# Optimization experiments

Measured on AMD Instinct MI355X. Metric: run time of the kernel, lower is better.

Reference implementation:

```python
import jax, jax.numpy as jnp
import numpy as np

NUM_NODES_G1 = 60000
NUM_NODES_G2 = 50000
NUM_REL = 16
NUM_BASES = 4
DIM = 128  # node_dim == hidden_dim == final_dim
L_COMMON = 100


def _concept_layer(x, edge_index):
    # Gather-based concept propagation: x_i <- x_i + mean_{j in N(i)} x_j
    src, dst = edge_index[0], edge_index[1]
    n = x.shape[0]
    agg = jax.ops.segment_sum(x[src], dst, num_segments=n)
    deg = jax.ops.segment_sum(jnp.ones((src.shape[0],), x.dtype), dst, num_segments=n)
    return x + agg / jnp.clip(deg, 1.0)[:, None]


def _rgcn_layer(x, edge_index, edge_type, basis, comp, root, bias):
    # Basis-decomposed RGCN: out_i = x_i @ root + bias + sum_r (1/|N_i^r|) sum_{j in N_i^r} x_j @ W_r,
    # W_r = sum_b comp[r,b] * basis[b]. Reorder: scatter comp-weighted x[src] per basis, then one GEMM per basis.
    src, dst = edge_index[0], edge_index[1]
    n = x.shape[0]
    e = src.shape[0]
    seg = dst * NUM_REL + edge_type  # per-(node, relation) bucket
    cnt = jax.ops.segment_sum(jnp.ones((e,), x.dtype), seg, num_segments=n * NUM_REL)
    norm = 1.0 / jnp.clip(cnt, 1.0)
    coef = comp[edge_type] * norm[seg][:, None]  # [E, B]
    xsrc = x[src]  # [E, D] -- dominant gather traffic
    out = x @ root + bias
    for b in range(NUM_BASES):  # small fixed loop over bases
        agg_b = jax.ops.segment_sum(xsrc * coef[:, b:b + 1], dst, num_segments=n)
        out = out + agg_b @ basis[b]
    return out


def setup_inputs() -> dict:
    key = jax.random.key(0)
    ks = jax.random.split(key, 16)
    e2, e1 = 800000, 800000
    return {
        "edge_index_g2": jax.random.randint(ks[0], (2, e2), 0, NUM_NODES_G2),
        "edge_type_g2": jax.random.randint(ks[1], (e2,), 0, NUM_REL),
        "edge_index_g1": jax.random.randint(ks[2], (2, e1), 0, NUM_NODES_G1),
        "left_common": jax.random.randint(ks[3], (L_COMMON,), 0, NUM_NODES_G1),
        "all_node_embedding": jax.random.normal(ks[4], (NUM_NODES_G1, DIM), jnp.float32),
        "basis1": jax.random.normal(ks[5], (NUM_BASES, DIM, DIM), jnp.float32) * 0.05,
        "comp1": jax.random.normal(ks[6], (NUM_REL, NUM_BASES), jnp.float32),
        "root1": jax.random.normal(ks[7], (DIM, DIM), jnp.float32) * 0.05,
        "bias1": jnp.zeros((DIM,), jnp.float32),
        "basis2": jax.random.normal(ks[8], (NUM_BASES, DIM, DIM), jnp.float32) * 0.05,
        "comp2": jax.random.normal(ks[9], (NUM_REL, NUM_BASES), jnp.float32),
        "root2": jax.random.normal(ks[10], (DIM, DIM), jnp.float32) * 0.05,
        "bias2": jnp.zeros((DIM,), jnp.float32),
        "weights": jax.random.uniform(ks[11], (DIM, 1), jnp.float32),
    }


def reference(edge_index_g2, edge_type_g2, edge_index_g1, left_common,
              all_node_embedding, basis1, comp1, root1, bias1,
              basis2, comp2, root2, bias2, weights):
    x_g1 = jax.nn.relu(_concept_layer(all_node_embedding, edge_index_g1))
    x = x_g1[:NUM_NODES_G2]
    x = _rgcn_layer(x, edge_index_g2, edge_type_g2, basis1, comp1, root1, bias1)
    x = jax.nn.relu(x)  # relu_use == 1
    x_g2 = _rgcn_layer(x, edge_index_g2, edge_type_g2, basis2, comp2, root2, bias2)
    ty = x_g1[left_common]  # [L, D]
    # mul_def outer elementwise product followed by matmul with weights collapses to one contraction:
    # logits[n,l] = sum_d x_g2[n,d] * ty[l,d] * w[d]
    logits = jnp.einsum('nd,ld,d->nl', x_g2, ty, weights[:, 0])
    return jax.nn.softmax(logits, axis=1)
```

## Files before the change

### kernel.cpp

```cpp
#include <hip/hip_runtime.h>
#include <hip/hip_bf16.h>
#include <math.h>

#define N1 60000
#define N2 50000
#define DIM 128
#define NREL 16
#define NB 4
#define LCOM 100
#define LPAD 112
#define NPART 8

typedef __attribute__((ext_vector_type(8))) short short8;
typedef __attribute__((ext_vector_type(4))) float f32x4;
typedef __attribute__((ext_vector_type(4))) _Float16 half4;
typedef __attribute__((ext_vector_type(8))) _Float16 half8;

__device__ __forceinline__ float bf2f(unsigned short u) {
    union { unsigned int i; float f; } c; c.i = ((unsigned int)u) << 16; return c.f;
}
__device__ __forceinline__ unsigned short f2bf(float f) {
    union { float f; unsigned int i; } c; c.f = f;
    unsigned int r = c.i + 0x7FFF + ((c.i >> 16) & 1);
    return (unsigned short)(r >> 16);
}
__device__ __forceinline__ void split8(float4 a, float4 b, short8& h, short8& l) {
    float f[8] = {a.x, a.y, a.z, a.w, b.x, b.y, b.z, b.w};
#pragma unroll
    for (int j = 0; j < 8; j++) {
        unsigned short hh = f2bf(f[j]);
        h[j] = (short)hh;
        l[j] = (short)f2bf(f[j] - bf2f(hh));
    }
}

__global__ __launch_bounds__(256) void k_prelude(
        const int* __restrict__ ei1, int E1, int* __restrict__ deg1, int HB1,
        const int* __restrict__ ei2, int E2, int* __restrict__ deg2, int HB2,
        const float* __restrict__ root1, const float* __restrict__ basis1,
        unsigned short* __restrict__ Wh1, unsigned short* __restrict__ Wl1,
        const float* __restrict__ root2, const float* __restrict__ basis2,
        unsigned short* __restrict__ Wh2, unsigned short* __restrict__ Wl2, int PB,
        const float* __restrict__ emb, _Float16* __restrict__ embh, int n4) {
    int b = blockIdx.x;
    if (b < HB1) {
        int e0 = b * 1024 + threadIdx.x;
#pragma unroll
        for (int j = 0; j < 4; j++) {
            int e = e0 + j * 256;
            if (e < E1) atomicAdd(deg1 + __builtin_nontemporal_load(ei1 + E1 + e), 1);
        }
    } else if (b < HB1 + HB2) {
        int e0 = (b - HB1) * 1024 + threadIdx.x;
#pragma unroll
        for (int j = 0; j < 4; j++) {
            int e = e0 + j * 256;
            if (e < E2) atomicAdd(deg2 + __builtin_nontemporal_load(ei2 + E2 + e), 1);
        }
    } else if (b < HB1 + HB2 + PB) {
        int t = (b - HB1 - HB2) * 256 + threadIdx.x;
        if (t < 2 * 640 * 128) {
            int which = t >= 640 * 128;
            int tt = which ? t - 640 * 128 : t;
            const float* root = which ? root2 : root1;
            const float* basis = which ? basis2 : basis1;
            unsigned short* Wh = which ? Wh2 : Wh1;
            unsigned short* Wl = which ? Wl2 : Wl1;
            int k = tt >> 7, n = tt & 127;
            float v = (k < 128) ? root[k * 128 + n] : basis[(k - 128) * 128 + n];
            unsigned short h = f2bf(v);
            Wh[n * 640 + k] = h;
            Wl[n * 640 + k] = f2bf(v - bf2f(h));
        }
    } else {
        int i = (b - HB1 - HB2 - PB) * 256 + threadIdx.x;
        if (i < n4) {
            float4 v = ((const float4*)emb)[i];
            half4 o = {(_Float16)v.x, (_Float16)v.y, (_Float16)v.z, (_Float16)v.w};
            ((half4*)embh)[i] = o;
        }
    }
}

__global__ __launch_bounds__(256) void k_scan_p1m(const int* __restrict__ inA, int nA, int nbA,
                                                  int* __restrict__ bsumA,
                                                  const int* __restrict__ inB, int nB,
                                                  int* __restrict__ bsumB) {
    __shared__ int red[256];
    const int* in; int n; int* bsum; int b;
    if ((int)blockIdx.x < nbA) { in = inA; n = nA; bsum = bsumA; b = blockIdx.x; }
    else { in = inB; n = nB; bsum = bsumB; b = blockIdx.x - nbA; }
    int base = b * 1024;
    int tid = threadIdx.x;
    int s = 0;
#pragma unroll
    for (int j = 0; j < 4; j++) {
        int i = base + tid * 4 + j;
        if (i < n) s += in[i];
    }
    red[tid] = s;
    __syncthreads();
    for (int d = 128; d; d >>= 1) {
        if (tid < d) red[tid] += red[tid + d];
        __syncthreads();
    }
    if (tid == 0) bsum[b] = red[0];
}

__global__ __launch_bounds__(64) void k_scan_p2m(const int* __restrict__ bsumA, int* __restrict__ boffA,
                                                 int* __restrict__ offA, int nbA, int nA,
                                                 const int* __restrict__ bsumB, int* __restrict__ boffB,
                                                 int* __restrict__ offB, int nbB, int nB) {
    __shared__ int s[64];
    const int* bsum; int* boff; int* off; int nb; int n;
    if (blockIdx.x == 0) { bsum = bsumA; boff = boffA; off = offA; nb = nbA; n = nA; }
    else { bsum = bsumB; boff = boffB; off = offB; nb = nbB; n = nB; }
    int tid = threadIdx.x;
    int v = (tid < nb) ? bsum[tid] : 0;
    s[tid] = v;
    __syncthreads();
    for (int d = 1; d < 64; d <<= 1) {
        int t = (tid >= d) ? s[tid - d] : 0;
        __syncthreads();
        s[tid] += t;
        __syncthreads();
    }
    if (tid < nb) boff[tid] = s[tid] - v;
    if (tid == 63) off[n] = s[63];
}

__global__ __launch_bounds__(256) void k_scan_p3m(const int* __restrict__ inA, const int* __restrict__ boffA,
                                                  int* __restrict__ offA, int* __restrict__ curA,
                                                  int nA, int nbA,
                                                  const int* __restrict__ inB, const int* __restrict__ boffB,
                                                  int* __restrict__ offB, int* __restrict__ curB, int nB) {
    __shared__ int red[256];
    const int* in; const int* boff; int* off; int* cur; int n; int b;
    if ((int)blockIdx.x < nbA) { in = inA; boff = boffA; off = offA; cur = curA; n = nA; b = blockIdx.x; }
    else { in = inB; boff = boffB; off = offB; cur = curB; n = nB; b = blockIdx.x - nbA; }
    int base = b * 1024;
    int tid = threadIdx.x;
    int v[4];
    int s = 0;
#pragma unroll
    for (int j = 0; j < 4; j++) {
        int i = base + tid * 4 + j;
        v[j] = (i < n) ? in[i] : 0;
        s += v[j];
    }
    red[tid] = s;
    __syncthreads();
    for (int d = 1; d < 256; d <<= 1) {
        int t = (tid >= d) ? red[tid - d] : 0;
        __syncthreads();
        red[tid] += t;
        __syncthreads();
    }
    int run = boff[b] + red[tid] - s;
#pragma unroll
    for (int j = 0; j < 4; j++) {
        int i = base + tid * 4 + j;
        if (i < n) {
            off[i] = run; cur[i] = run;
            run += v[j];
        }
    }
}

__global__ __launch_bounds__(256) void k_scat(const int* __restrict__ ei1, int E1,
                                              int* __restrict__ cur1, int* __restrict__ elist1, int G1) {
    int p = blockIdx.x & (NPART - 1);
    int c = blockIdx.x >> 3;
    const int W = (N1 + NPART - 1) / NPART;
    int lo = p * W, hi = min(lo + W, N1);
    int chunk = (E1 + G1 - 1) / G1;
    int e0 = c * chunk, e1 = min(e0 + chunk, E1);
    for (int base = e0; base < e1; base += 1024) {
        int d[4], s[4]; bool ok[4];
#pragma unroll
        for (int j = 0; j < 4; j++) {
            int e = base + threadIdx.x + j * 256;
            bool inb = e < e1;
            d[j] = inb ? __builtin_nontemporal_load(ei1 + E1 + e) : -1;
            s[j] = inb ? __builtin_nontemporal_load(ei1 + e) : 0;
            ok[j] = inb && d[j] >= lo && d[j] < hi;
        }
#pragma unroll
        for (int j = 0; j < 4; j++) {
            if (ok[j]) {
                int pos = atomicAdd(cur1 + d[j], 1);
                elist1[pos] = s[j];
            }
        }
    }
}

__global__ __launch_bounds__(256) void k_mix(
        const _Float16* __restrict__ embh, const float* __restrict__ emb,
        const int* __restrict__ off1, const int* __restrict__ elist1,
        float* __restrict__ xg1, _Float16* __restrict__ xg1h, int CONC_B,
        const int* __restrict__ ei2, const int* __restrict__ et2, int E2,
        int* __restrict__ cur2, int* __restrict__ elist2, int G2,
        const int* __restrict__ lc, const float* __restrict__ w,
        unsigned short* __restrict__ tyh, unsigned short* __restrict__ tyl) {
    int b = blockIdx.x;
    int SC2B = NPART * G2;
    if (b < SC2B) {
        int p = b & (NPART - 1);
        int c = b >> 3;
        const int W = (N2 + NPART - 1) / NPART;
        int lo = p * W, hi = min(lo + W, N2);
        int chunk = (E2 + G2 - 1) / G2;
        int e0 = c * chunk, e1 = min(e0 + chunk, E2);
        for (int base = e0; base < e1; base += 1024) {
            int d[4], s[4], t[4]; bool ok[4];
#pragma unroll
            for (int j = 0; j < 4; j++) {
                int e = base + threadIdx.x + j * 256;
                bool inb = e < e1;
                d[j] = inb ? __builtin_nontemporal_load(ei2 + E2 + e) : -1;
                s[j] = inb ? __builtin_nontemporal_load(ei2 + e) : 0;
                t[j] = inb ? __builtin_nontemporal_load(et2 + e) : 0;
                ok[j] = inb && d[j] >= lo && d[j] < hi;
            }
#pragma unroll
            for (int j = 0; j < 4; j++) {
                if (ok[j]) {
                    int pos = atomicAdd(cur2 + d[j], 1);
                    elist2[pos] = (s[j] << 4) | t[j];
                }
            }
        }
    } else if (b < SC2B + CONC_B) {
        int node = (b - SC2B) * 4 + (threadIdx.x >> 6);
        int lane = threadIdx.x & 63;
        if (node >= N2) return;
        int quad = lane >> 4, d8 = (lane & 15) * 8;
        int s0 = off1[node], s1 = off1[node + 1];
        float acc[8] = {};
        int i = s0;
        for (; i + 8 <= s1; i += 8) {
            int sa = elist1[i + quad];
            int sb = elist1[i + 4 + quad];
            half8 ha = *(const half8*)(embh + (size_t)sa * DIM + d8);
            half8 hb = *(const half8*)(embh + (size_t)sb * DIM + d8);
#pragma unroll
            for (int j = 0; j < 8; j++) acc[j] += (float)ha[j] + (float)hb[j];
        }
        if (i + 4 <= s1) {
            int sa = elist1[i + quad];
            half8 ha = *(const half8*)(embh + (size_t)sa * DIM + d8);
#pragma unroll
            for (int j = 0; j < 8; j++) acc[j] += (float)ha[j];
            i += 4;
        }
        if (i < s1) {
            int e = i + quad;
            bool ok = e < s1;
            int s = elist1[ok ? e : i];
            half8 hv = *(const half8*)(embh + (size_t)s * DIM + d8);
            if (ok) {
#pragma unroll
                for (int j = 0; j < 8; j++) acc[j] += (float)hv[j];
            }
        }
#pragma unroll
        for (int j = 0; j < 8; j++) {
            acc[j] += __shfl_xor(acc[j], 16, 64);
            acc[j] += __shfl_xor(acc[j], 32, 64);
        }
        if (quad == 0) {
            float inv = 1.0f / (float)max(s1 - s0, 1);
            const float* ep = emb + (size_t)node * DIM + d8;
            float4 e0 = *(const float4*)(ep);
            float4 e1 = *(const float4*)(ep + 4);
            float o[8];
            o[0] = fmaxf(e0.x + acc[0] * inv, 0.f);
            o[1] = fmaxf(e0.y + acc[1] * inv, 0.f);
            o[2] = fmaxf(e0.z + acc[2] * inv, 0.f);
            o[3] = fmaxf(e0.w + acc[3] * inv, 0.f);
            o[4] = fmaxf(e1.x + acc[4] * inv, 0.f);
            o[5] = fmaxf(e1.y + acc[5] * inv, 0.f);
            o[6] = fmaxf(e1.z + acc[6] * inv, 0.f);
            o[7] = fmaxf(e1.w + acc[7] * inv, 0.f);
            float4 w0 = {o[0], o[1], o[2], o[3]};
            float4 w1 = {o[4], o[5], o[6], o[7]};
            *(float4*)(xg1 + (size_t)node * DIM + d8) = w0;
            *(float4*)(xg1 + (size_t)node * DIM + d8 + 4) = w1;
            half8 oh;
#pragma unroll
            for (int j = 0; j < 8; j++) oh[j] = (_Float16)o[j];
            *(half8*)(xg1h + (size_t)node * DIM + d8) = oh;
        }
    } else {
        if (threadIdx.x >= 64) return;
        int l = b - SC2B - CONC_B;
        int lane = threadIdx.x;
        int d0 = lane * 2;
        if (l >= LCOM) {
            ushort2 z = {0, 0};
            *(ushort2*)(tyh + (size_t)l * 128 + d0) = z;
            *(ushort2*)(tyl + (size_t)l * 128 + d0) = z;
            return;
        }
        int row = lc[l];
        int s0 = off1[row], s1 = off1[row + 1];
        float2 acc = {0.f, 0.f};
        for (int i = s0; i < s1; i++) {
            int s = elist1[i];
            float2 v = *(const float2*)(emb + (size_t)s * DIM + lane * 2);
            acc.x += v.x; acc.y += v.y;
        }
        float inv = 1.0f / (float)max(s1 - s0, 1);
        float2 e = *(const float2*)(emb + (size_t)row * DIM + lane * 2);
        float v0 = fmaxf(e.x + acc.x * inv, 0.f) * w[d0];
        float v1 = fmaxf(e.y + acc.y * inv, 0.f) * w[d0 + 1];
        unsigned short h0 = f2bf(v0), h1 = f2bf(v1);
        ushort2 hh = {h0, h1};
        ushort2 ll = {f2bf(v0 - bf2f(h0)), f2bf(v1 - bf2f(h1))};
        *(ushort2*)(tyh + (size_t)l * 128 + d0) = hh;
        *(ushort2*)(tyl + (size_t)l * 128 + d0) = ll;
    }
}

__global__ __launch_bounds__(256) void k_rgcn_gather(const _Float16* __restrict__ xh,
                                                     const int* __restrict__ off,
                                                     const int* __restrict__ elist,
                                                     const float* __restrict__ comp,
                                                     float* __restrict__ agg, int n) {
    __shared__ float scomp[NREL * NB];
    __shared__ float nrmlds[4][NREL];
    if (threadIdx.x < NREL * NB) scomp[threadIdx.x] = comp[threadIdx.x];
    __syncthreads();
    int nb = threadIdx.x >> 6;
    int node = blockIdx.x * 4 + nb;
    int lane = threadIdx.x & 63;
    if (node >= n) return;
    int s0 = off[node], s1 = off[node + 1];
    unsigned long long c0 = 0, c1 = 0;
    for (int i = s0 + lane; i < s1; i += 64) {
        int t = elist[i] & 15;
        if (t < 8) c0 += 1ull << (8 * t); else c1 += 1ull << (8 * (t - 8));
    }
#pragma unroll
    for (int o = 32; o; o >>= 1) {
        c0 += __shfl_xor(c0, o, 64);
        c1 += __shfl_xor(c1, o, 64);
    }
    if (lane < NREL) {
        unsigned int c = (lane < 8) ? (unsigned int)((c0 >> (8 * lane)) & 255)
                                    : (unsigned int)((c1 >> (8 * (lane - 8))) & 255);
        nrmlds[nb][lane] = 1.0f / (float)max(c, 1u);
    }
    int quad = lane >> 4, d8 = (lane & 15) * 8;
    float a[4][8] = {};
#define RGE(P, GATE)                                                           \
    {                                                                          \
        int s_ = (P) >> 4, t_ = (P) & 15;                                      \
        float nr_ = nrmlds[nb][t_] * (GATE);                                   \
        float4 cf_ = *(const float4*)(scomp + t_ * 4);                         \
        half8 hv_ = *(const half8*)(xh + (size_t)s_ * DIM + d8);               \
        float c0_ = cf_.x * nr_, c1_ = cf_.y * nr_;                            \
        float c2_ = cf_.z * nr_, c3_ = cf_.w * nr_;                            \
        _Pragma("unroll")                                                      \
        for (int j = 0; j < 8; j++) {                                          \
            float v_ = (float)hv_[j];                                          \
            a[0][j] = fmaf(c0_, v_, a[0][j]);                                  \
            a[1][j] = fmaf(c1_, v_, a[1][j]);                                  \
            a[2][j] = fmaf(c2_, v_, a[2][j]);                                  \
            a[3][j] = fmaf(c3_, v_, a[3][j]);                                  \
        }                                                                      \
    }
    int i = s0;
    for (; i + 8 <= s1; i += 8) {
        int pa = elist[i + quad];
        int pb = elist[i + 4 + quad];
        RGE(pa, 1.0f);
        RGE(pb, 1.0f);
    }
    if (i + 4 <= s1) {
        int pa = elist[i + quad];
        RGE(pa, 1.0f);
        i += 4;
    }
    if (i < s1) {
        int e = i + quad;
        bool ok = e < s1;
        int pa = elist[ok ? e : i];
        RGE(pa, ok ? 1.0f : 0.0f);
    }
#undef RGE
#pragma unroll
    for (int bb = 0; bb < 4; bb++)
#pragma unroll
        for (int j = 0; j < 8; j++) {
            a[bb][j] += __shfl_xor(a[bb][j], 16, 64);
            a[bb][j] += __shfl_xor(a[bb][j], 32, 64);
        }
    if (quad == 0) {
        float* o = agg + (size_t)node * (NB * DIM) + d8;
#pragma unroll
        for (int bb = 0; bb < 4; bb++) {
            float4 v0 = {a[bb][0], a[bb][1], a[bb][2], a[bb][3]};
            float4 v1 = {a[bb][4], a[bb][5], a[bb][6], a[bb][7]};
            *(float4*)(o + bb * DIM) = v0;
            *(float4*)(o + bb * DIM + 4) = v1;
        }
    }
}

#define LDSK 40
__global__ __launch_bounds__(256) void k_gemm(const float* __restrict__ x,
                                              const float* __restrict__ agg,
                                              const unsigned short* __restrict__ Wh,
                                              const unsigned short* __restrict__ Wl,
                                              const float* __restrict__ bias,
                                              float* __restrict__ out,
                                              _Float16* __restrict__ out_h, int relu) {
    __shared__ __align__(16) short Ah[128 * LDSK];
    __shared__ __align__(16) short Al[128 * LDSK];
    __shared__ __align__(16) short Bh[128 * LDSK];
    __shared__ __align__(16) short Bl[128 * LDSK];
    int tid = threadIdx.x;
    int lane = tid & 63, wid = tid >> 6;
    int wave_m = wid >> 1, wave_n = wid & 1;
    int l15 = lane & 15, quad = lane >> 4;
    int row0 = blockIdx.x * 128;

    int srow = tid >> 1, skh = (tid & 1) * 16;

    f32x4 acc[4][4] = {};
    for (int k0 = 0; k0 < 640; k0 += 32) {
        {
            int rg = row0 + srow;
            float4 q0 = {0, 0, 0, 0}, q1 = q0, q2 = q0, q3 = q0;
            if (rg < N2) {
                const float* src = (k0 < 128) ? (x + (size_t)rg * 128 + k0 + skh)
                                              : (agg + (size_t)rg * 512 + (k0 - 128) + skh);
                q0 = *(const float4*)(src + 0);
                q1 = *(const float4*)(src + 4);
                q2 = *(const float4*)(src + 8);
                q3 = *(const float4*)(src + 12);
            }
            short8 h0, l0, h1, l1;
            split8(q0, q1, h0, l0);
            split8(q2, q3, h1, l1);
            *(short8*)(&Ah[srow * LDSK + skh]) = h0;
            *(short8*)(&Ah[srow * LDSK + skh + 8]) = h1;
            *(short8*)(&Al[srow * LDSK + skh]) = l0;
            *(short8*)(&Al[srow * LDSK + skh + 8]) = l1;
        }
        {
            const unsigned short* sh = Wh + (size_t)srow * 640 + k0 + skh;
            const unsigned short* sl = Wl + (size_t)srow * 640 + k0 + skh;
            *(short8*)(&Bh[srow * LDSK + skh]) = *(const short8*)(sh);
            *(short8*)(&Bh[srow * LDSK + skh + 8]) = *(const short8*)(sh + 8);
            *(short8*)(&Bl[srow * LDSK + skh]) = *(const short8*)(sl);
            *(short8*)(&Bl[srow * LDSK + skh + 8]) = *(const short8*)(sl + 8);
        }
        __syncthreads();
        short8 ah[4], al[4], bh[4], bl[4];
#pragma unroll
        for (int i = 0; i < 4; i++) {
            int ro = (wave_m * 64 + i * 16 + l15) * LDSK + quad * 8;
            ah[i] = *(const short8*)(&Ah[ro]);
            al[i] = *(const short8*)(&Al[ro]);
        }
#pragma unroll
        for (int j = 0; j < 4; j++) {
            int ro = (wave_n * 64 + j * 16 + l15) * LDSK + quad * 8;
            bh[j] = *(const short8*)(&Bh[ro]);
            bl[j] = *(const short8*)(&Bl[ro]);
        }
#pragma unroll
        for (int i = 0; i < 4; i++)
#pragma unroll
            for (int j = 0; j < 4; j++) {
                acc[i][j] = __builtin_amdgcn_mfma_f32_16x16x32_bf16(al[i], bh[j], acc[i][j], 0, 0, 0);
                acc[i][j] = __builtin_amdgcn_mfma_f32_16x16x32_bf16(ah[i], bl[j], acc[i][j], 0, 0, 0);
                acc[i][j] = __builtin_amdgcn_mfma_f32_16x16x32_bf16(ah[i], bh[j], acc[i][j], 0, 0, 0);
            }
        __syncthreads();
    }
#pragma unroll
    for (int j = 0; j < 4; j++) {
        int gcol = wave_n * 64 + j * 16 + l15;
        float bv = bias[gcol];
#pragma unroll
        for (int i = 0; i < 4; i++) {
            int grow_base = row0 + wave_m * 64 + i * 16 + quad * 4;
#pragma unroll
            for (int r = 0; r < 4; r++) {
                int grow = grow_base + r;
                if (grow >= N2) continue;
                float v = acc[i][j][r] + bv;
                if (relu) v = fmaxf(v, 0.f);
                out[(size_t)grow * 128 + gcol] = v;
                if (out_h) out_h[(size_t)grow * 128 + gcol] = (_Float16)v;
            }
        }
    }
}

__global__ __launch_bounds__(256) void k_logits(const float* __restrict__ h2,
                                                const unsigned short* __restrict__ tyh,
                                                const unsigned short* __restrict__ tyl,
                                                float* __restrict__ out, int M) {
    int wid = threadIdx.x >> 6, lane = threadIdx.x & 63;
    int l15 = lane & 15, quad = lane >> 4;
    int row0w = blockIdx.x * 64 + wid * 16;
    int arow = min(row0w + l15, M - 1);
    f32x4 acc[7] = {};
#pragma unroll
    for (int k0 = 0; k0 < 128; k0 += 32) {
        const float* ap = h2 + (size_t)arow * 128 + k0 + quad * 8;
        float4 q0 = *(const float4*)(ap);
        float4 q1 = *(const float4*)(ap + 4);
        short8 ah, al;
        split8(q0, q1, ah, al);
#pragma unroll
        for (int j = 0; j < 7; j++) {
            size_t bo = (size_t)(j * 16 + l15) * 128 + k0 + quad * 8;
            short8 bh = *(const short8*)(tyh + bo);
            short8 bl = *(const short8*)(tyl + bo);
            acc[j] = __builtin_amdgcn_mfma_f32_16x16x32_bf16(al, bh, acc[j], 0, 0, 0);
            acc[j] = __builtin_amdgcn_mfma_f32_16x16x32_bf16(ah, bl, acc[j], 0, 0, 0);
            acc[j] = __builtin_amdgcn_mfma_f32_16x16x32_bf16(ah, bh, acc[j], 0, 0, 0);
        }
    }
    bool v6 = (l15 < LCOM - 96);
#pragma unroll
    for (int r = 0; r < 4; r++) {
        int grow = row0w + quad * 4 + r;
        float m = -INFINITY;
#pragma unroll
        for (int j = 0; j < 6; j++) m = fmaxf(m, acc[j][r]);
        if (v6) m = fmaxf(m, acc[6][r]);
        m = fmaxf(m, __shfl_xor(m, 8, 64));
        m = fmaxf(m, __shfl_xor(m, 4, 64));
        m = fmaxf(m, __shfl_xor(m, 2, 64));
        m = fmaxf(m, __shfl_xor(m, 1, 64));
        float e[7];
        float s = 0.f;
#pragma unroll
        for (int j = 0; j < 6; j++) { e[j] = __expf(acc[j][r] - m); s += e[j]; }
        e[6] = v6 ? __expf(acc[6][r] - m) : 0.f;
        s += e[6];
        s += __shfl_xor(s, 8, 64);
        s += __shfl_xor(s, 4, 64);
        s += __shfl_xor(s, 2, 64);
        s += __shfl_xor(s, 1, 64);
        float inv = 1.0f / s;
        if (grow < M) {
#pragma unroll
            for (int j = 0; j < 6; j++) out[(size_t)grow * LCOM + j * 16 + l15] = e[j] * inv;
            if (v6) out[(size_t)grow * LCOM + 96 + l15] = e[6] * inv;
        }
    }
}

extern "C" void kernel_launch(void* const* d_in, const int* in_sizes, int n_in,
                              void* d_out, int out_size, void* d_ws, size_t ws_size,
                              hipStream_t stream) {
    const int* ei2 = (const int*)d_in[0];
    const int* et2 = (const int*)d_in[1];
    const int* ei1 = (const int*)d_in[2];
    const int* lc = (const int*)d_in[3];
    const float* emb = (const float*)d_in[4];
    const float* basis1 = (const float*)d_in[5];
    const float* comp1 = (const float*)d_in[6];
    const float* root1 = (const float*)d_in[7];
    const float* bias1 = (const float*)d_in[8];
    const float* basis2 = (const float*)d_in[9];
    const float* comp2 = (const float*)d_in[10];
    const float* root2 = (const float*)d_in[11];
    const float* bias2 = (const float*)d_in[12];
    const float* wts = (const float*)d_in[13];
    float* out = (float*)d_out;
    int E2 = in_sizes[0] / 2, E1 = in_sizes[2] / 2;

    float* ws = (float*)d_ws;
    float* xg1 = ws;
    float* h1 = xg1 + 6400000;
    float* agg = h1 + 6400000;
    _Float16* emb_h = (_Float16*)(agg + 25600000);
    unsigned short* tyh = (unsigned short*)(emb_h + 7680000);
    unsigned short* tyl = tyh + LPAD * 128;
    unsigned short* Wh1 = tyl + LPAD * 128;
    unsigned short* Wl1 = Wh1 + 81920;
    unsigned short* Wh2 = Wl1 + 81920;
    unsigned short* Wl2 = Wh2 + 81920;
    int* ipool = (int*)(Wl2 + 81920);
    int* deg1 = ipool;
    int* deg2 = deg1 + 60000;
    int* off1 = deg2 + 50000;
    int* cur1 = off1 + 60001;
    int* elist1 = cur1 + 60000;
    int* off2 = elist1 + 800000;
    int* cur2 = off2 + 50001;
    int* elist2 = cur2 + 50000;
    int* bsum1 = elist2 + 800000;
    int* boff1 = bsum1 + 64;
    int* bsum2 = boff1 + 64;
    int* boff2 = bsum2 + 64;
    _Float16* xg1_h = (_Float16*)h1;
    _Float16* h1_h = emb_h;
    float* h2 = xg1;

    const int NB1 = (N1 + 1023) / 1024;
    const int NB2 = (N2 + 1023) / 1024;
    const int HB1 = (E1 + 1023) / 1024;
    const int HB2 = (E2 + 1023) / 1024;
    const int PB = (2 * 640 * 128) / 256;
    const int CB = (N1 * DIM / 4 + 255) / 256;
    const int CONC_B = (N2 + 3) / 4;
    const int G1 = 128, G2 = 128;
    const int SC2B = NPART * G2;

    hipMemsetAsync(deg1, 0, (60000 + 50000) * sizeof(int), stream);

    k_prelude<<<HB1 + HB2 + PB + CB, 256, 0, stream>>>(
        ei1, E1, deg1, HB1, ei2, E2, deg2, HB2,
        root1, basis1, Wh1, Wl1, root2, basis2, Wh2, Wl2, PB,
        emb, emb_h, N1 * DIM / 4);

    k_scan_p1m<<<NB1 + NB2, 256, 0, stream>>>(deg1, N1, NB1, bsum1, deg2, N2, bsum2);
    k_scan_p2m<<<2, 64, 0, stream>>>(bsum1, boff1, off1, NB1, N1, bsum2, boff2, off2, NB2, N2);
    k_scan_p3m<<<NB1 + NB2, 256, 0, stream>>>(deg1, boff1, off1, cur1, N1, NB1,
                                              deg2, boff2, off2, cur2, N2);

    k_scat<<<NPART * G1, 256, 0, stream>>>(ei1, E1, cur1, elist1, G1);

    k_mix<<<SC2B + CONC_B + LPAD, 256, 0, stream>>>(
        emb_h, emb, off1, elist1, xg1, xg1_h, CONC_B,
        ei2, et2, E2, cur2, elist2, G2,
        lc, wts, tyh, tyl);

    k_rgcn_gather<<<CONC_B, 256, 0, stream>>>(xg1_h, off2, elist2, comp1, agg, N2);
    k_gemm<<<(N2 + 127) / 128, 256, 0, stream>>>(xg1, agg, Wh1, Wl1, bias1, h1, h1_h, 1);

    k_rgcn_gather<<<CONC_B, 256, 0, stream>>>(h1_h, off2, elist2, comp2, agg, N2);
    k_gemm<<<(N2 + 127) / 128, 256, 0, stream>>>(h1, agg, Wh2, Wl2, bias2, h2, (_Float16*)nullptr, 0);

    k_logits<<<(N2 + 63) / 64, 256, 0, stream>>>(h2, tyh, tyl, out, N2);
}
```

Measured before the change: 554.2 us.

## Replace global atomic degree histogram with partitioned LDS histograms per edge chunk

Degree counting moves from global atomics to per-block shared-memory histograms. Each block owns one node-range partition and one edge chunk, and writes a partial count slice to scratch reusing the agg buffer. The scan's first pass then sums the NC partial slices to produce the final degrees, which removes the memset and global atomic contention. In exchange every block reads its whole edge chunk (each edge is read NPART times), the scan pass reads more data, and fewer blocks run the histogram.

```diff
diff --git a/kernel.cpp b/kernel.cpp
--- a/kernel.cpp
+++ b/kernel.cpp
@@ -10,6 +10,7 @@
 #define LCOM 100
 #define LPAD 112
 #define NPART 8
+#define NC 16
 
 typedef __attribute__((ext_vector_type(8))) short short8;
 typedef __attribute__((ext_vector_type(4))) float f32x4;
@@ -35,30 +36,50 @@
 }
 
 __global__ __launch_bounds__(256) void k_prelude(
-        const int* __restrict__ ei1, int E1, int* __restrict__ deg1, int HB1,
-        const int* __restrict__ ei2, int E2, int* __restrict__ deg2, int HB2,
+        const int* __restrict__ ei1, int E1, int* __restrict__ degs1,
+        const int* __restrict__ ei2, int E2, int* __restrict__ degs2,
         const float* __restrict__ root1, const float* __restrict__ basis1,
         unsigned short* __restrict__ Wh1, unsigned short* __restrict__ Wl1,
         const float* __restrict__ root2, const float* __restrict__ basis2,
         unsigned short* __restrict__ Wh2, unsigned short* __restrict__ Wl2, int PB,
         const float* __restrict__ emb, _Float16* __restrict__ embh, int n4) {
+    __shared__ int hist[7500];
     int b = blockIdx.x;
-    if (b < HB1) {
-        int e0 = b * 1024 + threadIdx.x;
-#pragma unroll
-        for (int j = 0; j < 4; j++) {
-            int e = e0 + j * 256;
-            if (e < E1) atomicAdd(deg1 + __builtin_nontemporal_load(ei1 + E1 + e), 1);
-        }
-    } else if (b < HB1 + HB2) {
-        int e0 = (b - HB1) * 1024 + threadIdx.x;
-#pragma unroll
-        for (int j = 0; j < 4; j++) {
-            int e = e0 + j * 256;
-            if (e < E2) atomicAdd(deg2 + __builtin_nontemporal_load(ei2 + E2 + e), 1);
-        }
-    } else if (b < HB1 + HB2 + PB) {
-        int t = (b - HB1 - HB2) * 256 + threadIdx.x;
+    const int HB = NPART * NC;
+    if (b < 2 * HB) {
+        int isg2 = b >= HB;
+        int bb = isg2 ? b - HB : b;
+        int p = bb & (NPART - 1);
+        int c = bb >> 3;
+        const int* dsts = isg2 ? ei2 + E2 : ei1 + E1;
+        int E = isg2 ? E2 : E1;
+        int N = isg2 ? N2 : N1;
+        int* degs = isg2 ? degs2 : degs1;
+        const int W = (N + NPART - 1) / NPART;
+        int lo = p * W, hi = min(lo + W, N);
+        int span = hi - lo;
+        for (int i = threadIdx.x; i < span; i += 256) hist[i] = 0;
+        __syncthreads();
+        int chunk = (E + NC - 1) / NC;
+        int e0 = c * chunk, e1 = min(e0 + chunk, E);
+        for (int base = e0; base < e1; base += 1024) {
+            int d[4]; bool ok[4];
+#pragma unroll
+            for (int j = 0; j < 4; j++) {
+                int e = base + threadIdx.x + j * 256;
+                bool inb = e < e1;
+                d[j] = inb ? __builtin_nontemporal_load(dsts + e) : -1;
+                ok[j] = inb && d[j] >= lo && d[j] < hi;
+            }
+#pragma unroll
+            for (int j = 0; j < 4; j++)
+                if (ok[j]) atomicAdd(&hist[d[j] - lo], 1);
+        }
+        __syncthreads();
+        int* slice = degs + (size_t)c * N + lo;
+        for (int i = threadIdx.x; i < span; i += 256) slice[i] = hist[i];
+    } else if (b < 2 * HB + PB) {
+        int t = (b - 2 * HB) * 256 + threadIdx.x;
         if (t < 2 * 640 * 128) {
             int which = t >= 640 * 128;
             int tt = which ? t - 640 * 128 : t;
@@ -73,7 +94,7 @@
             Wl[n * 640 + k] = f2bf(v - bf2f(h));
         }
     } else {
-        int i = (b - HB1 - HB2 - PB) * 256 + threadIdx.x;
+        int i = (b - 2 * HB - PB) * 256 + threadIdx.x;
         if (i < n4) {
             float4 v = ((const float4*)emb)[i];
             half4 o = {(_Float16)v.x, (_Float16)v.y, (_Float16)v.z, (_Float16)v.w};
@@ -82,21 +103,27 @@
     }
 }
 
-__global__ __launch_bounds__(256) void k_scan_p1m(const int* __restrict__ inA, int nA, int nbA,
-                                                  int* __restrict__ bsumA,
-                                                  const int* __restrict__ inB, int nB,
-                                                  int* __restrict__ bsumB) {
+__global__ __launch_bounds__(256) void k_scan_p1m(const int* __restrict__ degsA, int* __restrict__ degA,
+                                                  int nA, int nbA, int* __restrict__ bsumA,
+                                                  const int* __restrict__ degsB, int* __restrict__ degB,
+                                                  int nB, int* __restrict__ bsumB) {
     __shared__ int red[256];
-    const int* in; int n; int* bsum; int b;
-    if ((int)blockIdx.x < nbA) { in = inA; n = nA; bsum = bsumA; b = blockIdx.x; }
-    else { in = inB; n = nB; bsum = bsumB; b = blockIdx.x - nbA; }
+    const int* degs; int* deg; int n; int* bsum; int b;
+    if ((int)blockIdx.x < nbA) { degs = degsA; deg = degA; n = nA; bsum = bsumA; b = blockIdx.x; }
+    else { degs = degsB; deg = degB; n = nB; bsum = bsumB; b = blockIdx.x - nbA; }
     int base = b * 1024;
     int tid = threadIdx.x;
     int s = 0;
 #pragma unroll
     for (int j = 0; j < 4; j++) {
         int i = base + tid * 4 + j;
-        if (i < n) s += in[i];
+        if (i < n) {
+            int v = 0;
+#pragma unroll
+            for (int c = 0; c < NC; c++) v += degs[(size_t)c * n + i];
+            deg[i] = v;
+            s += v;
+        }
     }
     red[tid] = s;
     __syncthreads();
@@ -603,28 +630,27 @@
     int* boff1 = bsum1 + 64;
     int* bsum2 = boff1 + 64;
     int* boff2 = bsum2 + 64;
+    int* degs1 = (int*)agg;
+    int* degs2 = degs1 + NC * N1;
     _Float16* xg1_h = (_Float16*)h1;
     _Float16* h1_h = emb_h;
     float* h2 = xg1;
 
     const int NB1 = (N1 + 1023) / 1024;
     const int NB2 = (N2 + 1023) / 1024;
-    const int HB1 = (E1 + 1023) / 1024;
-    const int HB2 = (E2 + 1023) / 1024;
     const int PB = (2 * 640 * 128) / 256;
     const int CB = (N1 * DIM / 4 + 255) / 256;
     const int CONC_B = (N2 + 3) / 4;
     const int G1 = 128, G2 = 128;
     const int SC2B = NPART * G2;
 
-    hipMemsetAsync(deg1, 0, (60000 + 50000) * sizeof(int), stream);
-
-    k_prelude<<<HB1 + HB2 + PB + CB, 256, 0, stream>>>(
-        ei1, E1, deg1, HB1, ei2, E2, deg2, HB2,
+    k_prelude<<<2 * NPART * NC + PB + CB, 256, 0, stream>>>(
+        ei1, E1, degs1, ei2, E2, degs2,
         root1, basis1, Wh1, Wl1, root2, basis2, Wh2, Wl2, PB,
         emb, emb_h, N1 * DIM / 4);
 
-    k_scan_p1m<<<NB1 + NB2, 256, 0, stream>>>(deg1, N1, NB1, bsum1, deg2, N2, bsum2);
+    k_scan_p1m<<<NB1 + NB2, 256, 0, stream>>>(degs1, deg1, N1, NB1, bsum1,
+                                              degs2, deg2, N2, bsum2);
     k_scan_p2m<<<2, 64, 0, stream>>>(bsum1, boff1, off1, NB1, N1, bsum2, boff2, off2, NB2, N2);
     k_scan_p3m<<<NB1 + NB2, 256, 0, stream>>>(deg1, boff1, off1, cur1, N1, NB1,
                                               deg2, boff2, off2, cur2, N2);
```

Result: faster. 532.2 us (-4.0%).
